# Kernel tuning notes

Hardware: AMD Instinct MI355X
Metric: run time of the kernel (lower is better)

## Reference

```python
import jax, jax.numpy as jnp
import numpy as np
from jax import lax

NJ = 14
COL = 14
SIGMA = 1.0
RADIUS = 4  # scipy gaussian_filter: truncate=4.0 * sigma=1.0 -> radius 4


def _gauss_kernel():
    x = np.arange(-RADIUS, RADIUS + 1, dtype=np.float32)
    w = np.exp(-0.5 * x * x / (SIGMA * SIGMA))
    w /= w.sum()
    return jnp.asarray(w)


def _blur(delta):
    # separable gaussian with scipy mode='reflect' (== np.pad 'symmetric')
    B, J, H, W = delta.shape
    w = _gauss_kernel()
    p = jnp.pad(delta, ((0, 0), (0, 0), (RADIUS, RADIUS), (RADIUS, RADIUS)), mode='symmetric')
    lhs = p.reshape(B * J, 1, H + 2 * RADIUS, W + 2 * RADIUS)
    kh = w.reshape(1, 1, 2 * RADIUS + 1, 1)
    kw = w.reshape(1, 1, 1, 2 * RADIUS + 1)
    dn = ('NCHW', 'OIHW', 'NCHW')
    y = lax.conv_general_dilated(lhs, kh, (1, 1), 'VALID', dimension_numbers=dn)
    y = lax.conv_general_dilated(y, kw, (1, 1), 'VALID', dimension_numbers=dn)
    return y.reshape(B, J, H, W)


def setup_inputs() -> dict:
    key = jax.random.key(0)
    k1, k2, k3, k4 = jax.random.split(key, 4)
    B = 8192
    o = jax.random.normal(k1, (B, 2 * NJ, COL, COL), jnp.float32)
    h = jax.random.uniform(k2, (B, NJ, COL, COL), jnp.float32)
    t = jax.random.uniform(k3, (B, NJ, 2), jnp.float32)
    vis = jax.random.randint(k4, (B, NJ), 0, 2).astype(jnp.float32)
    v = jnp.repeat(vis[..., None], 2, axis=-1)  # visibility duplicated over (x,y)
    return {"o": o, "h": h, "t": t, "v": v}


def reference(o, h, t, v):
    B = h.shape[0]
    scale = 1.0 / float(COL)
    f32 = jnp.float32

    # argmax coordinate extraction from predicted heatmaps
    argmax = jnp.argmax(h.reshape(B, NJ, COL * COL), axis=-1)  # [B,Nj]
    yC = argmax // COL
    xC = argmax - yC * COL
    bidx = jnp.arange(B)[:, None]
    jidx = jnp.arange(NJ)[None, :]

    h_peak = h[bidx, jidx, yC, xC]                 # [B,Nj]
    cond = h_peak > 0.5
    ox = o[bidx, jidx, yC, xC]                     # offset channels 0..Nj-1
    oy = o[bidx, jidx + NJ, yC, xC]                # offset channels Nj..2Nj-1
    x0 = jnp.where(cond, (ox + xC.astype(f32)) * scale, 0.0)
    x1 = jnp.where(cond, (oy + yC.astype(f32)) * scale, 0.0)
    x = jnp.stack([x0, x1], axis=-1)               # [B,Nj,2]

    # per-joint gaussian target heatmap (only where visible)
    ti = t * COL
    xi = jnp.clip(ti[..., 0].astype(jnp.int32), 0, COL - 1)
    yi = jnp.clip(ti[..., 1].astype(jnp.int32), 0, COL - 1)
    visf = (v[..., 0].astype(jnp.int32) == 1).astype(f32)  # [B,Nj]
    delta = jnp.zeros((B, NJ, COL, COL), f32).at[bidx, jidx, yi, xi].set(visf)
    g = _blur(delta)
    mn = g.min(axis=(-2, -1), keepdims=True)
    mx = g.max(axis=(-2, -1), keepdims=True)
    denom = jnp.where(mx > mn, mx - mn, 1.0)
    tt = jnp.where(visf[..., None, None] > 0, (g - mn) / denom, 0.0)

    # heatmap loss; original zeroes only ROW 0 of diff for invisible joints
    diff1 = h - tt
    row0 = diff1[:, :, 0:1, :] * visf[:, :, None, None]
    diff1 = jnp.concatenate([row0, diff1[:, :, 1:, :]], axis=2)
    N1 = v.sum() / 2.0
    d1 = jnp.sum(diff1 * diff1) / N1

    # coordinate loss
    diff2 = (x - t) * v
    d2 = jnp.sum(diff2 * diff2) / N1  # N2 == N1 in the original
    return d1 + d2
```

## Files before the change

### kernel.cpp

```cpp
#include <hip/hip_runtime.h>

#define NJ    14
#define TILE  196
#define BLK   256
#define JPB   64

__device__ __forceinline__ float gtap(int d) {
  const int d2 = d * d;
  const float e = exp2f(-0.72134752044448169f * (float)d2);
  return (d2 <= 16) ? e : 0.0f;
}

__device__ __forceinline__ float uresp(int p, int pk) {
  float s = gtap(p - pk);
  if (p <= 3)  s += gtap(p + pk + 1);
  if (p >= 10) s += gtap(27 - p - pk);
  return s;
}

__device__ __forceinline__ float wave_sum(float x) {
#pragma unroll
  for (int off = 32; off >= 1; off >>= 1) x += __shfl_xor(x, off);
  return x;
}

template<int K>
__device__ __forceinline__ void accum_part(const float4* __restrict__ hp,
    const float (&uy)[14], const float (&ux)[14],
    float& bm, int& bi, float& sh2, float& cross, float& q0)
{
  const int NI = (K == 0) ? 13 : 12;
#pragma unroll
  for (int i = 0; i < NI; ++i) {
    const int f = 4 * i + K;
    const float4 q = hp[f];
    const float qa[4] = {q.x, q.y, q.z, q.w};
#pragma unroll
    for (int c = 0; c < 4; ++c) {
      const int idx = 4 * f + c;
      const int y = idx / 14;
      const int x = idx - 14 * y;
      const float hv = qa[c];
      if (hv > bm) { bm = hv; bi = idx; }
      sh2 = fmaf(hv, hv, sh2);
      if (y == 0) q0 = fmaf(hv, hv, q0);
      cross = fmaf(hv, uy[y] * ux[x], cross);
    }
  }
}

__global__ __launch_bounds__(BLK, 4) void joint_kernel(
    const float* __restrict__ o, const float* __restrict__ h,
    const float* __restrict__ t, const float* __restrict__ v,
    float* __restrict__ part, int njoint, int nblocks)
{
  __shared__ float sm_bm[4][JPB];
  __shared__ int   sm_bi[4][JPB];
  __shared__ float sm_s2[4][JPB];
  __shared__ float sm_cr[4][JPB];
  __shared__ float sm_q0[4][JPB];

  const int lane = threadIdx.x & 63;
  const int wid  = threadIdx.x >> 6;
  const int jg   = blockIdx.x * JPB + lane;
  const bool valid = jg < njoint;

  float uy[14], ux[14];
  float bm = -3.0e38f; int bi = 0;
  float sh2 = 0.0f, cross = 0.0f, q0 = 0.0f;
  float2 tv = make_float2(0.0f, 0.0f);
  int xi = 0, yi = 0;

  if (valid) {
    tv = ((const float2*)t)[jg];
    xi = min(max((int)(tv.x * 14.0f), 0), 13);
    yi = min(max((int)(tv.y * 14.0f), 0), 13);
#pragma unroll
    for (int p = 0; p < 14; ++p) { uy[p] = uresp(p, yi); ux[p] = uresp(p, xi); }

    const float4* hp = (const float4*)(h + (size_t)jg * TILE);
    switch (wid) {
      case 0: accum_part<0>(hp, uy, ux, bm, bi, sh2, cross, q0); break;
      case 1: accum_part<1>(hp, uy, ux, bm, bi, sh2, cross, q0); break;
      case 2: accum_part<2>(hp, uy, ux, bm, bi, sh2, cross, q0); break;
      default: accum_part<3>(hp, uy, ux, bm, bi, sh2, cross, q0); break;
    }
  }

  sm_bm[wid][lane] = bm;  sm_bi[wid][lane] = bi;
  sm_s2[wid][lane] = sh2; sm_cr[wid][lane] = cross; sm_q0[wid][lane] = q0;
  __syncthreads();

  float s_acc = 0.0f, n_acc = 0.0f;
  if (wid == 0) {
    float Bm = sm_bm[0][lane]; int Bi = sm_bi[0][lane];
    float S2 = sm_s2[0][lane], Cr = sm_cr[0][lane], Q0 = sm_q0[0][lane];
#pragma unroll
    for (int w = 1; w < 4; ++w) {
      const float m = sm_bm[w][lane]; const int i = sm_bi[w][lane];
      if (m > Bm || (m == Bm && i < Bi)) { Bm = m; Bi = i; }
      S2 += sm_s2[w][lane]; Cr += sm_cr[w][lane]; Q0 += sm_q0[w][lane];
    }

    if (valid) {
      const float2 vv = ((const float2*)v)[jg];
      const bool vis = ((int)vv.x) == 1;

      float Sy2 = 0.0f, Sx2 = 0.0f;
#pragma unroll
      for (int p = 0; p < 14; ++p) {
        Sy2 = fmaf(uy[p], uy[p], Sy2);
        Sx2 = fmaf(ux[p], ux[p], Sx2);
      }
      const float maxy = 1.0f + gtap(2 * yi + 1) + gtap(27 - 2 * yi);
      const float maxx = 1.0f + gtap(2 * xi + 1) + gtap(27 - 2 * xi);
      const float inv = vis ? (1.0f / (maxy * maxx)) : 0.0f;

      float s = S2 - 2.0f * inv * Cr + inv * inv * Sy2 * Sx2;
      if (!vis) s -= Q0;

      const int b = jg / NJ;
      const int j = jg - b * NJ;
      const int yC = Bi / 14;
      const int xC = Bi - 14 * yC;
      const size_t ob = ((size_t)b * (2 * NJ) + j) * TILE + (size_t)Bi;
      const float ox = o[ob];
      const float oy = o[ob + (size_t)NJ * TILE];
      const bool cond = Bm > 0.5f;
      const float sc = 1.0f / 14.0f;
      const float px = cond ? (ox + (float)xC) * sc : 0.0f;
      const float py = cond ? (oy + (float)yC) * sc : 0.0f;
      const float d0 = (px - tv.x) * vv.x;
      const float d1 = (py - tv.y) * vv.y;
      s += d0 * d0 + d1 * d1;

      s_acc = s;
      n_acc = vv.x + vv.y;
    }

    s_acc = wave_sum(s_acc);
    n_acc = wave_sum(n_acc);
    if (lane == 0) {
      part[blockIdx.x]           = s_acc;
      part[nblocks + blockIdx.x] = n_acc;
    }
  }
}

__global__ __launch_bounds__(BLK) void finalize_kernel(
    const float* __restrict__ part, float* __restrict__ out, int nblocks)
{
  float s = 0.0f, n = 0.0f;
  for (int i = threadIdx.x; i < nblocks; i += BLK) {
    s += part[i];
    n += part[nblocks + i];
  }
  s = wave_sum(s);
  n = wave_sum(n);
  __shared__ float rs[4], rn[4];
  const int lane = threadIdx.x & 63, wid = threadIdx.x >> 6;
  if (lane == 0) { rs[wid] = s; rn[wid] = n; }
  __syncthreads();
  if (threadIdx.x == 0) {
    const float S = rs[0] + rs[1] + rs[2] + rs[3];
    const float N = rn[0] + rn[1] + rn[2] + rn[3];
    out[0] = S / (0.5f * N);
  }
}

extern "C" void kernel_launch(void* const* d_in, const int* in_sizes, int n_in,
                              void* d_out, int out_size, void* d_ws, size_t ws_size,
                              hipStream_t stream)
{
  const float* o = (const float*)d_in[0];
  const float* h = (const float*)d_in[1];
  const float* t = (const float*)d_in[2];
  const float* v = (const float*)d_in[3];
  const int njoint = in_sizes[1] / TILE;
  const int nblocks = (njoint + JPB - 1) / JPB;

  float* part = (float*)d_ws;
  joint_kernel<<<nblocks, BLK, 0, stream>>>(o, h, t, v, part, njoint, nblocks);
  finalize_kernel<<<1, BLK, 0, stream>>>(part, (float*)d_out, nblocks);
}
```

Measured before the change: 34.59 us.

## Stage heatmap tiles into LDS with direct global-to-LDS async loads

Each block now copies its 64 heatmap tiles into shared memory using coalesced global_load_lds 16-byte transfers. Lanes then read their strided tile slices from LDS instead of making uncoalesced per-lane float4 global loads. The staging buffer is reused for the cross-wave reduction, and launch bounds drop to 3 blocks per SM to fit about 50KB of LDS. This trades lower occupancy, LDS bank conflicts from the 196-float stride, and an extra barrier for coalesced DRAM access.

```diff
diff --git a/kernel.cpp b/kernel.cpp
--- a/kernel.cpp
+++ b/kernel.cpp
@@ -4,6 +4,10 @@
 #define TILE  196
 #define BLK   256
 #define JPB   64
+#define STAGE_DW (JPB * TILE)
+
+typedef __attribute__((address_space(1))) const void g_void;
+typedef __attribute__((address_space(3))) void lds_void;
 
 __device__ __forceinline__ float gtap(int d) {
   const int d2 = d * d;
@@ -49,36 +53,51 @@
   }
 }
 
-__global__ __launch_bounds__(BLK, 4) void joint_kernel(
+__global__ __launch_bounds__(BLK, 3) void joint_kernel(
     const float* __restrict__ o, const float* __restrict__ h,
     const float* __restrict__ t, const float* __restrict__ v,
     float* __restrict__ part, int njoint, int nblocks)
 {
-  __shared__ float sm_bm[4][JPB];
-  __shared__ int   sm_bi[4][JPB];
-  __shared__ float sm_s2[4][JPB];
-  __shared__ float sm_cr[4][JPB];
-  __shared__ float sm_q0[4][JPB];
-
-  const int lane = threadIdx.x & 63;
-  const int wid  = threadIdx.x >> 6;
+  __shared__ __align__(16) float lds[STAGE_DW];
+
+  const int tid  = threadIdx.x;
+  const int lane = tid & 63;
+  const int wid  = tid >> 6;
   const int jg   = blockIdx.x * JPB + lane;
   const bool valid = jg < njoint;
 
+  const int ntile = min(JPB, njoint - blockIdx.x * JPB);
+  const int n4 = ntile * 49;
+  const float* gbase = h + (size_t)blockIdx.x * JPB * TILE;
+#pragma unroll
+  for (int i = 0; i < 13; ++i) {
+    const int idx = i * BLK + tid;
+    if (idx < n4) {
+      __builtin_amdgcn_global_load_lds(
+          (g_void*)(gbase + (size_t)idx * 4),
+          (lds_void*)&lds[idx * 4],
+          16, 0, 0);
+    }
+  }
+
   float uy[14], ux[14];
-  float bm = -3.0e38f; int bi = 0;
-  float sh2 = 0.0f, cross = 0.0f, q0 = 0.0f;
   float2 tv = make_float2(0.0f, 0.0f);
   int xi = 0, yi = 0;
-
   if (valid) {
     tv = ((const float2*)t)[jg];
     xi = min(max((int)(tv.x * 14.0f), 0), 13);
     yi = min(max((int)(tv.y * 14.0f), 0), 13);
 #pragma unroll
     for (int p = 0; p < 14; ++p) { uy[p] = uresp(p, yi); ux[p] = uresp(p, xi); }
-
-    const float4* hp = (const float4*)(h + (size_t)jg * TILE);
+  }
+
+  asm volatile("s_waitcnt vmcnt(0)" ::: "memory");
+  __syncthreads();
+
+  float bm = -3.0e38f; int bi = 0;
+  float sh2 = 0.0f, cross = 0.0f, q0 = 0.0f;
+  if (valid) {
+    const float4* hp = (const float4*)&lds[lane * TILE];
     switch (wid) {
       case 0: accum_part<0>(hp, uy, ux, bm, bi, sh2, cross, q0); break;
       case 1: accum_part<1>(hp, uy, ux, bm, bi, sh2, cross, q0); break;
@@ -87,21 +106,29 @@
     }
   }
 
-  sm_bm[wid][lane] = bm;  sm_bi[wid][lane] = bi;
-  sm_s2[wid][lane] = sh2; sm_cr[wid][lane] = cross; sm_q0[wid][lane] = q0;
-  __syncthreads();
-
-  float s_acc = 0.0f, n_acc = 0.0f;
+  __syncthreads();
+  float* red = lds;
+  red[0 * BLK + tid] = bm;
+  ((int*)lds)[1 * BLK + tid] = bi;
+  red[2 * BLK + tid] = sh2;
+  red[3 * BLK + tid] = cross;
+  red[4 * BLK + tid] = q0;
+  __syncthreads();
+
   if (wid == 0) {
-    float Bm = sm_bm[0][lane]; int Bi = sm_bi[0][lane];
-    float S2 = sm_s2[0][lane], Cr = sm_cr[0][lane], Q0 = sm_q0[0][lane];
+    float Bm = red[lane]; int Bi = ((int*)lds)[BLK + lane];
+    float S2 = red[2 * BLK + lane], Cr = red[3 * BLK + lane], Q0 = red[4 * BLK + lane];
 #pragma unroll
     for (int w = 1; w < 4; ++w) {
-      const float m = sm_bm[w][lane]; const int i = sm_bi[w][lane];
+      const float m = red[w * 64 + lane];
+      const int   i = ((int*)lds)[BLK + w * 64 + lane];
       if (m > Bm || (m == Bm && i < Bi)) { Bm = m; Bi = i; }
-      S2 += sm_s2[w][lane]; Cr += sm_cr[w][lane]; Q0 += sm_q0[w][lane];
-    }
-
+      S2 += red[2 * BLK + w * 64 + lane];
+      Cr += red[3 * BLK + w * 64 + lane];
+      Q0 += red[4 * BLK + w * 64 + lane];
+    }
+
+    float s_acc = 0.0f, n_acc = 0.0f;
     if (valid) {
       const float2 vv = ((const float2*)v)[jg];
       const bool vis = ((int)vv.x) == 1;
```

Result: faster. 29.91 us (-13.5%).

## Persistent 256-block kernel with double-buffered async global-to-LDS heatmap staging

Applied to the files above, without the earlier changes.

Replaces the one-block-per-64-joints launch with a fixed grid of 256 persistent blocks, each processing 7 chunks of 64 joints. Heatmap tiles are copied into two LDS buffers with global_load_lds and explicit vmcnt waits, so the load of chunk k+2 overlaps compute on chunk k. t and v are staged into LDS up front. The grid size, chunk count and joint count are hardcoded (256*7*64 = B*NJ), so the kernel no longer checks bounds and only works for this input size. The larger LDS footprint lowers occupancy.

```diff
diff --git a/kernel.cpp b/kernel.cpp
--- a/kernel.cpp
+++ b/kernel.cpp
@@ -3,7 +3,14 @@
 #define NJ    14
 #define TILE  196
 #define BLK   256
-#define JPB   64
+#define JPC   64
+#define N4C   (JPC * 49)
+#define NCH   7
+#define JPB   (JPC * NCH)
+#define GRID  256
+
+typedef __attribute__((address_space(1))) const void g_void;
+typedef __attribute__((address_space(3))) void lds_void;
 
 __device__ __forceinline__ float gtap(int d) {
   const int d2 = d * d;
@@ -49,61 +56,105 @@
   }
 }
 
-__global__ __launch_bounds__(BLK, 4) void joint_kernel(
+__device__ __forceinline__ void stage_chunk(const float* __restrict__ h,
+    size_t jbase, int c, float* dst, int tid, int wid, int lane)
+{
+  const float* gsrc = h + (jbase + (size_t)c * JPC) * TILE;
+#pragma unroll
+  for (int i = 0; i < 12; ++i) {
+    const int idx = i * BLK + tid;
+    __builtin_amdgcn_global_load_lds(
+        (g_void*)(gsrc + (size_t)idx * 4),
+        (lds_void*)(dst + (size_t)idx * 4), 16, 0, 0);
+  }
+  if (wid == 0) {
+    const int idx = 12 * BLK + lane;
+    __builtin_amdgcn_global_load_lds(
+        (g_void*)(gsrc + (size_t)idx * 4),
+        (lds_void*)(dst + (size_t)idx * 4), 16, 0, 0);
+  }
+}
+
+__global__ __launch_bounds__(BLK) void joint_kernel(
     const float* __restrict__ o, const float* __restrict__ h,
     const float* __restrict__ t, const float* __restrict__ v,
-    float* __restrict__ part, int njoint, int nblocks)
-{
-  __shared__ float sm_bm[4][JPB];
-  __shared__ int   sm_bi[4][JPB];
-  __shared__ float sm_s2[4][JPB];
-  __shared__ float sm_cr[4][JPB];
-  __shared__ float sm_q0[4][JPB];
-
-  const int lane = threadIdx.x & 63;
-  const int wid  = threadIdx.x >> 6;
-  const int jg   = blockIdx.x * JPB + lane;
-  const bool valid = jg < njoint;
-
-  float uy[14], ux[14];
-  float bm = -3.0e38f; int bi = 0;
-  float sh2 = 0.0f, cross = 0.0f, q0 = 0.0f;
-  float2 tv = make_float2(0.0f, 0.0f);
-  int xi = 0, yi = 0;
-
-  if (valid) {
-    tv = ((const float2*)t)[jg];
-    xi = min(max((int)(tv.x * 14.0f), 0), 13);
-    yi = min(max((int)(tv.y * 14.0f), 0), 13);
+    float* __restrict__ part)
+{
+  __shared__ __align__(16) float bufA[N4C * 4];
+  __shared__ __align__(16) float bufB[N4C * 4];
+  __shared__ float pf[2][4][4][JPC];
+  __shared__ int   pib[2][4][JPC];
+  __shared__ __align__(16) float tlds[JPB * 2];
+  __shared__ __align__(16) float vlds[JPB * 2];
+
+  const int tid  = threadIdx.x;
+  const int lane = tid & 63;
+  const int wid  = tid >> 6;
+  const size_t jbase = (size_t)blockIdx.x * JPB;
+
+  if (tid < JPB * 2 / 4) {
+    __builtin_amdgcn_global_load_lds(
+        (g_void*)(t + jbase * 2 + (size_t)tid * 4), (lds_void*)&tlds[tid * 4], 16, 0, 0);
+    __builtin_amdgcn_global_load_lds(
+        (g_void*)(v + jbase * 2 + (size_t)tid * 4), (lds_void*)&vlds[tid * 4], 16, 0, 0);
+  }
+  stage_chunk(h, jbase, 0, bufA, tid, wid, lane);
+  stage_chunk(h, jbase, 1, bufB, tid, wid, lane);
+
+  float s_acc = 0.0f, n_acc = 0.0f;
+
+  for (int k = 0; k < NCH; ++k) {
+    if (k == NCH - 1)    asm volatile("s_waitcnt vmcnt(0)" ::: "memory");
+    else if (wid == 0)   asm volatile("s_waitcnt vmcnt(13)" ::: "memory");
+    else                 asm volatile("s_waitcnt vmcnt(12)" ::: "memory");
+    __builtin_amdgcn_s_barrier();
+    asm volatile("" ::: "memory");
+
+    const int jl = k * JPC + lane;
+    const float2 tv = *(const float2*)&tlds[jl * 2];
+    const int xi = min(max((int)(tv.x * 14.0f), 0), 13);
+    const int yi = min(max((int)(tv.y * 14.0f), 0), 13);
+    float uy[14], ux[14];
 #pragma unroll
     for (int p = 0; p < 14; ++p) { uy[p] = uresp(p, yi); ux[p] = uresp(p, xi); }
 
-    const float4* hp = (const float4*)(h + (size_t)jg * TILE);
+    const float* bsrc = (k & 1) ? bufB : bufA;
+    const float4* hp = (const float4*)(bsrc + lane * TILE);
+    float bm = -3.0e38f; int bi = 0;
+    float sh2 = 0.0f, cross = 0.0f, q0 = 0.0f;
     switch (wid) {
-      case 0: accum_part<0>(hp, uy, ux, bm, bi, sh2, cross, q0); break;
-      case 1: accum_part<1>(hp, uy, ux, bm, bi, sh2, cross, q0); break;
-      case 2: accum_part<2>(hp, uy, ux, bm, bi, sh2, cross, q0); break;
+      case 0:  accum_part<0>(hp, uy, ux, bm, bi, sh2, cross, q0); break;
+      case 1:  accum_part<1>(hp, uy, ux, bm, bi, sh2, cross, q0); break;
+      case 2:  accum_part<2>(hp, uy, ux, bm, bi, sh2, cross, q0); break;
       default: accum_part<3>(hp, uy, ux, bm, bi, sh2, cross, q0); break;
     }
-  }
-
-  sm_bm[wid][lane] = bm;  sm_bi[wid][lane] = bi;
-  sm_s2[wid][lane] = sh2; sm_cr[wid][lane] = cross; sm_q0[wid][lane] = q0;
-  __syncthreads();
-
-  float s_acc = 0.0f, n_acc = 0.0f;
-  if (wid == 0) {
-    float Bm = sm_bm[0][lane]; int Bi = sm_bi[0][lane];
-    float S2 = sm_s2[0][lane], Cr = sm_cr[0][lane], Q0 = sm_q0[0][lane];
-#pragma unroll
-    for (int w = 1; w < 4; ++w) {
-      const float m = sm_bm[w][lane]; const int i = sm_bi[w][lane];
-      if (m > Bm || (m == Bm && i < Bi)) { Bm = m; Bi = i; }
-      S2 += sm_s2[w][lane]; Cr += sm_cr[w][lane]; Q0 += sm_q0[w][lane];
-    }
-
-    if (valid) {
-      const float2 vv = ((const float2*)v)[jg];
+
+    const int par = k & 1;
+    pf[par][0][wid][lane] = bm;
+    pib[par][wid][lane]   = bi;
+    pf[par][1][wid][lane] = sh2;
+    pf[par][2][wid][lane] = cross;
+    pf[par][3][wid][lane] = q0;
+    asm volatile("s_waitcnt lgkmcnt(0)" ::: "memory");
+    __builtin_amdgcn_s_barrier();
+    asm volatile("" ::: "memory");
+
+    if (wid == 0) {
+      float Bm = pf[par][0][0][lane]; int Bi = pib[par][0][lane];
+      float S2 = pf[par][1][0][lane];
+      float Cr = pf[par][2][0][lane];
+      float Q0 = pf[par][3][0][lane];
+#pragma unroll
+      for (int w = 1; w < 4; ++w) {
+        const float m = pf[par][0][w][lane];
+        const int   i = pib[par][w][lane];
+        if (m > Bm || (m == Bm && i < Bi)) { Bm = m; Bi = i; }
+        S2 += pf[par][1][w][lane];
+        Cr += pf[par][2][w][lane];
+        Q0 += pf[par][3][w][lane];
+      }
+
+      const float2 vv = *(const float2*)&vlds[jl * 2];
       const bool vis = ((int)vv.x) == 1;
 
       float Sy2 = 0.0f, Sx2 = 0.0f;
@@ -119,6 +170,7 @@
       float s = S2 - 2.0f * inv * Cr + inv * inv * Sy2 * Sx2;
       if (!vis) s -= Q0;
 
+      const int jg = (int)jbase + jl;
       const int b = jg / NJ;
       const int j = jg - b * NJ;
       const int yC = Bi / 14;
@@ -134,34 +186,39 @@
       const float d1 = (py - tv.y) * vv.y;
       s += d0 * d0 + d1 * d1;
 
-      s_acc = s;
-      n_acc = vv.x + vv.y;
-    }
-
-    s_acc = wave_sum(s_acc);
-    n_acc = wave_sum(n_acc);
+      s_acc += s;
+      n_acc += vv.x + vv.y;
+      asm volatile("" : "+v"(s_acc), "+v"(n_acc));
+    }
+
+    if (k + 2 < NCH) {
+      stage_chunk(h, jbase, k + 2, (k & 1) ? bufB : bufA, tid, wid, lane);
+    }
+  }
+
+  if (wid == 0) {
+    const float S = wave_sum(s_acc);
+    const float N = wave_sum(n_acc);
     if (lane == 0) {
-      part[blockIdx.x]           = s_acc;
-      part[nblocks + blockIdx.x] = n_acc;
+      part[blockIdx.x]        = S;
+      part[GRID + blockIdx.x] = N;
     }
   }
 }
 
 __global__ __launch_bounds__(BLK) void finalize_kernel(
-    const float* __restrict__ part, float* __restrict__ out, int nblocks)
-{
-  float s = 0.0f, n = 0.0f;
-  for (int i = threadIdx.x; i < nblocks; i += BLK) {
-    s += part[i];
-    n += part[nblocks + i];
-  }
+    const float* __restrict__ part, float* __restrict__ out)
+{
+  const int tid = threadIdx.x;
+  float s = part[tid];
+  float n = part[GRID + tid];
   s = wave_sum(s);
   n = wave_sum(n);
   __shared__ float rs[4], rn[4];
-  const int lane = threadIdx.x & 63, wid = threadIdx.x >> 6;
+  const int lane = tid & 63, wid = tid >> 6;
   if (lane == 0) { rs[wid] = s; rn[wid] = n; }
   __syncthreads();
-  if (threadIdx.x == 0) {
+  if (tid == 0) {
     const float S = rs[0] + rs[1] + rs[2] + rs[3];
     const float N = rn[0] + rn[1] + rn[2] + rn[3];
     out[0] = S / (0.5f * N);
@@ -176,10 +233,8 @@
   const float* h = (const float*)d_in[1];
   const float* t = (const float*)d_in[2];
   const float* v = (const float*)d_in[3];
-  const int njoint = in_sizes[1] / TILE;
-  const int nblocks = (njoint + JPB - 1) / JPB;
 
   float* part = (float*)d_ws;
-  joint_kernel<<<nblocks, BLK, 0, stream>>>(o, h, t, v, part, njoint, nblocks);
-  finalize_kernel<<<1, BLK, 0, stream>>>(part, (float*)d_out, nblocks);
-}
+  joint_kernel<<<GRID, BLK, 0, stream>>>(o, h, t, v, part);
+  finalize_kernel<<<1, BLK, 0, stream>>>(part, (float*)d_out);
+}
```

Result: no change. 35.28 us (+2.0%).
